# Performance work log

Hardware: AMD Instinct MI355X
Metric: run time of the kernel (lower is better)

Reference implementation:

```python
import jax, jax.numpy as jnp
import numpy as np

B, S, D, H = 4, 2048, 1024, 16
DK = D // H


def setup_inputs() -> dict:
    key = jax.random.key(0)
    ks = jax.random.split(key, 11)
    std = 1.0 / np.sqrt(D)
    mk = lambda k: jax.random.uniform(k, (D, D), jnp.float32, -std, std)
    mb = lambda k: jax.random.uniform(k, (D,), jnp.float32, -std, std)
    return {
        "query": jax.random.normal(ks[0], (B, S, D), jnp.float32),
        "key": jax.random.normal(ks[1], (B, S, D), jnp.float32),
        "value": jax.random.normal(ks[2], (B, S, D), jnp.float32),
        "Wq": mk(ks[3]), "bq": mb(ks[4]),
        "Wk": mk(ks[5]), "bk": mb(ks[6]),
        "Wv": mk(ks[7]), "bv": mb(ks[8]),
        "Wo": mk(ks[9]), "bo": mb(ks[10]),
    }


def reference(query, key, value, Wq, bq, Wk, bk, Wv, bv, Wo, bo):
    # Linear projections (torch Linear: x @ W.T + b)
    Q = query @ Wq.T + bq   # [B,S,D]
    K = key @ Wk.T + bk
    V = value @ Wv.T + bv
    # split heads -> [B,H,S,DK]
    Q = Q.reshape(B, S, H, DK).transpose(0, 2, 1, 3)
    K = K.reshape(B, S, H, DK).transpose(0, 2, 1, 3)
    V = V.reshape(B, S, H, DK).transpose(0, 2, 1, 3)
    scale = 1.0 / jnp.sqrt(jnp.asarray(DK, Q.dtype))
    scores = jnp.einsum("bhqd,bhkd->bhqk", Q, K) * scale  # [B,H,S,S]
    attn = jax.nn.softmax(scores, axis=-1)
    out = jnp.einsum("bhqk,bhkd->bhqd", attn, V)          # [B,H,S,DK]
    out = out.transpose(0, 2, 1, 3).reshape(B, S, D)       # [B,S,D]
    return out @ Wo.T + bo
```

## Files before the change

### kernel.cpp

```cpp
#include <hip/hip_runtime.h>
#include <hip/hip_bf16.h>
#include <stdint.h>


using f32x4  = __attribute__((ext_vector_type(4))) float;
using f32x16 = __attribute__((ext_vector_type(16))) float;
using s16x8  = __attribute__((ext_vector_type(8))) short;
using u16x8  = __attribute__((ext_vector_type(8))) unsigned short;
using u16x4  = __attribute__((ext_vector_type(4))) unsigned short;

#define MFMA16(a, b, c) __builtin_amdgcn_mfma_f32_16x16x32_bf16((a), (b), (c), 0, 0, 0)
#define MFMA32(a, b, c) __builtin_amdgcn_mfma_f32_32x32x16_bf16((a), (b), (c), 0, 0, 0)

#define GLL16(gptr, lptr)                                                      \
  __builtin_amdgcn_global_load_lds(                                            \
      (const __attribute__((address_space(1))) void*)(gptr),                   \
      (__attribute__((address_space(3))) void*)(lptr), 16, 0, 0)

__device__ __forceinline__ unsigned short f2bf(float f) {
  union { __hip_bfloat16 h; unsigned short u; } cv;
  cv.h = __float2bfloat16(f);
  return cv.u;
}

__device__ __forceinline__ unsigned int pkrne(float a, float b) {
  unsigned int ua = __builtin_bit_cast(unsigned int, a);
  unsigned int ub = __builtin_bit_cast(unsigned int, b);
  ua = ua + 0x7FFFu + ((ua >> 16) & 1u);
  ub = ub + 0x7FFFu + ((ub >> 16) & 1u);
  return __builtin_amdgcn_perm(ub, ua, 0x07060302u);
}

__device__ __forceinline__ float exp2a(float x) {
  return __builtin_amdgcn_exp2f(x);
}

__global__ __launch_bounds__(256) void cast_all_kernel(
    const float* __restrict__ wq, const float* __restrict__ wk,
    const float* __restrict__ wv, const float* __restrict__ wo,
    const float* __restrict__ xq, const float* __restrict__ xk,
    const float* __restrict__ xv, unsigned short* __restrict__ wbf,
    unsigned short* __restrict__ oxq, unsigned short* __restrict__ oxk,
    unsigned short* __restrict__ oxv) {
  const int job = blockIdx.y;
  const int i = blockIdx.x * 256 + threadIdx.x;
  const float* src;
  unsigned short* dst;
  size_t off;
  if (job < 4) {
    src = (job == 0) ? wq : (job == 1) ? wk : (job == 2) ? wv : wo;
    dst = wbf + (size_t)job * 1048576;
    off = (size_t)i;
  } else {
    const int xi = job - 4, z = xi >> 3, sl = xi & 7;
    src = (z == 0) ? xq : (z == 1) ? xk : xv;
    dst = (z == 0) ? oxq : (z == 1) ? oxk : oxv;
    off = (size_t)sl * 262144 + i;
  }
  float4 f = reinterpret_cast<const float4*>(src)[off];
  uint2 p;
  p.x = pkrne(f.x, f.y);
  p.y = pkrne(f.z, f.w);
  *reinterpret_cast<uint2*>(dst + off * 4) = p;
}

__global__ __launch_bounds__(256) void gemm_qkvv_kernel(
    const unsigned short* __restrict__ Xq, const unsigned short* __restrict__ Xk,
    const unsigned short* __restrict__ Xv, const unsigned short* __restrict__ wbf,
    const float* __restrict__ bq, const float* __restrict__ bk,
    const float* __restrict__ bv, unsigned short* __restrict__ Qh,
    unsigned short* __restrict__ Kh, unsigned short* __restrict__ Vh) {
  const int z = blockIdx.z;
  const unsigned short* Xbf = (z == 0) ? Xq : (z == 1) ? Xk : Xv;
  const unsigned short* W = wbf + (size_t)z * 1048576;
  const float* bias = (z == 0) ? bq : (z == 1) ? bk : bv;
  const float qscale = (z == 0) ? 0.18033688011112042f : 1.0f;

  __shared__ __align__(16) unsigned short Asm_[128 * 64];
  __shared__ __align__(16) unsigned short Bsm_[128 * 64];

  const int t = threadIdx.x;
  const int lane = t & 63, w = t >> 6;
  const int g = lane >> 4, c = lane & 15;
  const int wm = (w >> 1) * 64, wn = (w & 1) * 64;
  const int n0 = (blockIdx.y & 7) * 128;
  const int m0 = (blockIdx.x * 8 + (blockIdx.y >> 3)) * 128;

  f32x4 acc[4][4];
#pragma unroll
  for (int i = 0; i < 4; i++)
#pragma unroll
    for (int j = 0; j < 4; j++) acc[i][j] = (f32x4)0.0f;

  const int blr = lane >> 3;
  const int bgc = (lane & 7) ^ blr;

  for (int kt = 0; kt < 16; ++kt) {
    const int k0 = kt * 64;
    __syncthreads();
#pragma unroll
    for (int i = 0; i < 4; i++) {
      int ii = w * 4 + i;
      const unsigned short* ga = Xbf + (size_t)(m0 + ii * 8 + blr) * 1024 + k0 + bgc * 8;
      GLL16(ga, &Asm_[ii * 512]);
      const unsigned short* gb = W + (size_t)(n0 + ii * 8 + blr) * 1024 + k0 + bgc * 8;
      GLL16(gb, &Bsm_[ii * 512]);
    }
    __syncthreads();

#pragma unroll
    for (int ks = 0; ks < 2; ks++) {
      s16x8 af[4], bfr[4];
#pragma unroll
      for (int mt = 0; mt < 4; mt++) {
        int r = wm + mt * 16 + c;
        af[mt] = *reinterpret_cast<const s16x8*>(&Asm_[r * 64 + (((ks * 4 + g) ^ (c & 7)) << 3)]);
      }
#pragma unroll
      for (int nt = 0; nt < 4; nt++) {
        int r = wn + nt * 16 + c;
        bfr[nt] = *reinterpret_cast<const s16x8*>(&Bsm_[r * 64 + (((ks * 4 + g) ^ (c & 7)) << 3)]);
      }
      if (z == 2) {
#pragma unroll
        for (int nt = 0; nt < 4; nt++)
#pragma unroll
          for (int mt = 0; mt < 4; mt++)
            acc[nt][mt] = MFMA16(bfr[nt], af[mt], acc[nt][mt]);
      } else {
#pragma unroll
        for (int mt = 0; mt < 4; mt++)
#pragma unroll
          for (int nt = 0; nt < 4; nt++)
            acc[mt][nt] = MFMA16(af[mt], bfr[nt], acc[mt][nt]);
      }
    }
  }

  if (z == 2) {
#pragma unroll
    for (int nt = 0; nt < 4; nt++)
#pragma unroll
      for (int mt = 0; mt < 4; mt++) {
        int m = m0 + wm + mt * 16 + c;
        int b = m >> 11, s = m & 2047;
#pragma unroll
        for (int r = 0; r < 4; r++) {
          int n = n0 + wn + nt * 16 + g * 4 + r;
          int h = n >> 6, dk = n & 63;
          Vh[(((size_t)b * 16 + h) * 64 + dk) * 2048 + s] =
              f2bf(acc[nt][mt][r] + bv[n]);
        }
      }
  } else {
    unsigned short* dst = (z == 0) ? Qh : Kh;
#pragma unroll
    for (int mt = 0; mt < 4; mt++)
#pragma unroll
      for (int nt = 0; nt < 4; nt++) {
        int n = n0 + wn + nt * 16 + c;
        float bb = bias[n];
        int h = n >> 6, dk = n & 63;
#pragma unroll
        for (int r = 0; r < 4; r++) {
          int m = m0 + wm + mt * 16 + g * 4 + r;
          int b = m >> 11, s = m & 2047;
          dst[(((size_t)b * 16 + h) * 2048 + s) * 64 + dk] =
              f2bf((acc[mt][nt][r] + bb) * qscale);
        }
      }
  }
}

__global__ __launch_bounds__(256) void gemm_out_kernel(
    const unsigned short* __restrict__ AO, const unsigned short* __restrict__ Wo,
    const float* __restrict__ bo, float* __restrict__ out) {
  __shared__ __align__(16) unsigned short Asm_[128 * 64];
  __shared__ __align__(16) unsigned short Bsm_[64 * 64];

  const int t = threadIdx.x;
  const int lane = t & 63, w = t >> 6;
  const int g = lane >> 4, c = lane & 15;
  const int wm = (w >> 1) * 64, wn = (w & 1) * 32;
  const int n0 = (blockIdx.y & 15) * 64;
  const int m0 = (blockIdx.x * 8 + (blockIdx.y >> 4)) * 128;

  f32x4 acc[4][2];
#pragma unroll
  for (int i = 0; i < 4; i++)
#pragma unroll
    for (int j = 0; j < 2; j++) acc[i][j] = (f32x4)0.0f;

  const int blr = lane >> 3;
  const int bgc = (lane & 7) ^ blr;

  for (int kt = 0; kt < 16; ++kt) {
    const int k0 = kt * 64;
    __syncthreads();
#pragma unroll
    for (int i = 0; i < 4; i++) {
      int ii = w * 4 + i;
      const unsigned short* ga = AO + (size_t)(m0 + ii * 8 + blr) * 1024 + k0 + bgc * 8;
      GLL16(ga, &Asm_[ii * 512]);
    }
#pragma unroll
    for (int i = 0; i < 2; i++) {
      int ii = w * 2 + i;
      const unsigned short* gb = Wo + (size_t)(n0 + ii * 8 + blr) * 1024 + k0 + bgc * 8;
      GLL16(gb, &Bsm_[ii * 512]);
    }
    __syncthreads();

#pragma unroll
    for (int ks = 0; ks < 2; ks++) {
      s16x8 af[4], bfr[2];
#pragma unroll
      for (int mt = 0; mt < 4; mt++) {
        int r = wm + mt * 16 + c;
        af[mt] = *reinterpret_cast<const s16x8*>(&Asm_[r * 64 + (((ks * 4 + g) ^ (c & 7)) << 3)]);
      }
#pragma unroll
      for (int nt = 0; nt < 2; nt++) {
        int r = wn + nt * 16 + c;
        bfr[nt] = *reinterpret_cast<const s16x8*>(&Bsm_[r * 64 + (((ks * 4 + g) ^ (c & 7)) << 3)]);
      }
#pragma unroll
      for (int mt = 0; mt < 4; mt++)
#pragma unroll
        for (int nt = 0; nt < 2; nt++)
          acc[mt][nt] = MFMA16(af[mt], bfr[nt], acc[mt][nt]);
    }
  }

#pragma unroll
  for (int mt = 0; mt < 4; mt++)
#pragma unroll
    for (int nt = 0; nt < 2; nt++) {
      int n = n0 + wn + nt * 16 + c;
      float bb = bo[n];
#pragma unroll
      for (int r = 0; r < 4; r++) {
        int m = m0 + wm + mt * 16 + g * 4 + r;
        out[(size_t)m * 1024 + n] = acc[mt][nt][r] + bb;
      }
    }
}

__global__ __launch_bounds__(512) void attn_kernel(
    const unsigned short* __restrict__ Qh, const unsigned short* __restrict__ Kh,
    const unsigned short* __restrict__ Vh, unsigned short* __restrict__ AO) {
  const int bh = blockIdx.x * 8 + (blockIdx.y >> 3);
  const int b = bh >> 4, h = bh & 15;
  const int q0 = (blockIdx.y & 7) * 256;
  const int t = threadIdx.x, lane = t & 63, w = t >> 6;
  const int lo = lane & 31, hi = lane >> 5;

  __shared__ __align__(16) unsigned short Ks[2][64 * 64];
  __shared__ __align__(16) unsigned short Vs[2][64 * 64];

  const size_t kvbase = (size_t)bh * 2048 * 64;

  s16x8 qb[4];
  {
    const unsigned short* qp = Qh + kvbase + (size_t)(q0 + w * 32 + lo) * 64;
#pragma unroll
    for (int ks = 0; ks < 4; ks++)
      qb[ks] = *reinterpret_cast<const s16x8*>(qp + ks * 16 + hi * 8);
  }

  s16x8 onesb;
  {
    uint4 u;
    u.x = 0x3F803F80u; u.y = 0x3F803F80u; u.z = 0x3F803F80u; u.w = 0x3F803F80u;
    onesb = *reinterpret_cast<const s16x8*>(&u);
  }

  f32x16 oacc[2], lacc;
  oacc[0] = (f32x16)0.0f; oacc[1] = (f32x16)0.0f; lacc = (f32x16)0.0f;

  const int srow = t >> 3;
  const int gch = (t & 7) ^ (srow & 7) ^ w;
  const unsigned short* Kg = Kh + kvbase + (size_t)srow * 64 + gch * 8;
  const unsigned short* Vg = Vh + kvbase + (size_t)srow * 2048 + gch * 8;

  const int rx0 = (lo & 7) ^ (lo >> 3);
  const int rx1 = (lo & 7) ^ (4 | (lo >> 3));

  GLL16(Kg, &Ks[0][w * 512]);
  GLL16(Vg, &Vs[0][w * 512]);
  __syncthreads();

  for (int it = 0; it < 32; ++it) {
    const int cur = it & 1;
    if (it < 31) {
      const int kv = (it + 1) * 64;
      GLL16(Kg + (size_t)kv * 64, &Ks[cur ^ 1][w * 512]);
      GLL16(Vg + kv, &Vs[cur ^ 1][w * 512]);
    }

    f32x16 st[2];
    st[0] = (f32x16)0.0f; st[1] = (f32x16)0.0f;
#pragma unroll
    for (int kb = 0; kb < 2; kb++) {
      const int rx = kb ? rx1 : rx0;
#pragma unroll
      for (int ks = 0; ks < 4; ks++) {
        s16x8 ka = *reinterpret_cast<const s16x8*>(
            &Ks[cur][(kb * 32 + lo) * 64 + (((ks * 2 + hi) ^ rx) << 3)]);
        st[kb] = MFMA32(ka, qb[ks], st[kb]);
      }
    }

    s16x8 pa[4];
#pragma unroll
    for (int kb = 0; kb < 2; kb++) {
      float e[16];
#pragma unroll
      for (int r = 0; r < 16; r++) e[r] = exp2a(st[kb][r]);
#pragma unroll
      for (int half = 0; half < 2; half++) {
        const float* eb = e + half * 8;
        unsigned int x1 = pkrne(eb[0], eb[1]);
        unsigned int x2 = pkrne(eb[2], eb[3]);
        unsigned int y1 = pkrne(eb[4], eb[5]);
        unsigned int y2 = pkrne(eb[6], eb[7]);
        asm volatile("v_permlane32_swap_b32 %0, %1" : "+v"(x1), "+v"(y1));
        asm volatile("v_permlane32_swap_b32 %0, %1" : "+v"(x2), "+v"(y2));
        uint4 u;
        u.x = x1; u.y = x2; u.z = y1; u.w = y2;
        pa[kb * 2 + half] = *reinterpret_cast<const s16x8*>(&u);
      }
    }

#pragma unroll
    for (int ks = 0; ks < 4; ks++) lacc = MFMA32(pa[ks], onesb, lacc);

#pragma unroll
    for (int ks = 0; ks < 4; ks++)
#pragma unroll
      for (int db = 0; db < 2; db++) {
        const int rx = db ? rx1 : rx0;
        s16x8 vb = *reinterpret_cast<const s16x8*>(
            &Vs[cur][(db * 32 + lo) * 64 + (((ks * 2 + hi) ^ rx) << 3)]);
        oacc[db] = MFMA32(pa[ks], vb, oacc[db]);
      }

    __syncthreads();
  }

#pragma unroll
  for (int r = 0; r < 16; r++) {
    float inv_r = 1.0f / lacc[r];
    int qr = (r & 3) + ((r >> 2) << 3) + (hi << 2);
    int srow_q = q0 + w * 32 + qr;
    size_t obase = ((size_t)b * 2048 + srow_q) * 1024 + (size_t)h * 64;
    AO[obase + lo]      = f2bf(oacc[0][r] * inv_r);
    AO[obase + 32 + lo] = f2bf(oacc[1][r] * inv_r);
  }
}

extern "C" void kernel_launch(void* const* d_in, const int* in_sizes, int n_in,
                              void* d_out, int out_size, void* d_ws, size_t ws_size,
                              hipStream_t stream) {
  const float* query = (const float*)d_in[0];
  const float* key   = (const float*)d_in[1];
  const float* value = (const float*)d_in[2];
  const float* Wq = (const float*)d_in[3];
  const float* bq = (const float*)d_in[4];
  const float* Wk = (const float*)d_in[5];
  const float* bk = (const float*)d_in[6];
  const float* Wv = (const float*)d_in[7];
  const float* bv = (const float*)d_in[8];
  const float* Wo = (const float*)d_in[9];
  const float* bo = (const float*)d_in[10];

  uint8_t* wsb = (uint8_t*)d_ws;
  unsigned short* wbf = (unsigned short*)wsb;
  unsigned short* Qh  = (unsigned short*)(wsb + 8388608);
  unsigned short* Kh  = (unsigned short*)(wsb + 8388608 + 16777216);
  unsigned short* Vh  = (unsigned short*)(wsb + 8388608 + 2 * 16777216);
  unsigned short* AO  = (unsigned short*)(wsb + 8388608 + 3 * 16777216);
  unsigned short* Xq = AO;
  unsigned short* Xk = (unsigned short*)d_out;
  unsigned short* Xv = (unsigned short*)d_out + 8388608;

  cast_all_kernel<<<dim3(1024, 28), dim3(256), 0, stream>>>(
      Wq, Wk, Wv, Wo, query, key, value, wbf, Xq, Xk, Xv);
  gemm_qkvv_kernel<<<dim3(8, 64, 3), dim3(256), 0, stream>>>(
      Xq, Xk, Xv, wbf, bq, bk, bv, Qh, Kh, Vh);
  attn_kernel<<<dim3(8, 64), dim3(512), 0, stream>>>(Qh, Kh, Vh, AO);
  gemm_out_kernel<<<dim3(8, 128), dim3(256), 0, stream>>>(
      AO, wbf + (size_t)3 * 1048576, bo, (float*)d_out);
}
```

Measured before the change: 206.9 us.

## Split attention KV range across two blocks and combine partial outputs

Attention now runs on a grid with a z dimension of 2. Each block processes half of the key/value sequence and writes an unnormalized bf16 partial output and its row sums into scratch buffers, which reuse the output and weight workspaces. A new combine kernel adds the two partials and divides by the summed row normalizers to produce the attention output. This doubles the number of blocks so more work can be in flight. The cost is an extra kernel launch, extra global memory traffic for the partials, and an additional bf16 rounding of the unnormalized partial outputs.

```diff
diff --git a/kernel.cpp b/kernel.cpp
--- a/kernel.cpp
+++ b/kernel.cpp
@@ -29,6 +29,10 @@
   ua = ua + 0x7FFFu + ((ua >> 16) & 1u);
   ub = ub + 0x7FFFu + ((ub >> 16) & 1u);
   return __builtin_amdgcn_perm(ub, ua, 0x07060302u);
+}
+
+__device__ __forceinline__ float bf2f(unsigned short u) {
+  return __builtin_bit_cast(float, (unsigned int)u << 16);
 }
 
 __device__ __forceinline__ float exp2a(float x) {
@@ -248,10 +252,12 @@
 
 __global__ __launch_bounds__(512) void attn_kernel(
     const unsigned short* __restrict__ Qh, const unsigned short* __restrict__ Kh,
-    const unsigned short* __restrict__ Vh, unsigned short* __restrict__ AO) {
+    const unsigned short* __restrict__ Vh, unsigned short* __restrict__ Opart,
+    float* __restrict__ lw) {
   const int bh = blockIdx.x * 8 + (blockIdx.y >> 3);
   const int b = bh >> 4, h = bh & 15;
   const int q0 = (blockIdx.y & 7) * 256;
+  const int kvh = blockIdx.z;
   const int t = threadIdx.x, lane = t & 63, w = t >> 6;
   const int lo = lane & 31, hi = lane >> 5;
 
@@ -286,16 +292,18 @@
   const int rx0 = (lo & 7) ^ (lo >> 3);
   const int rx1 = (lo & 7) ^ (4 | (lo >> 3));
 
-  GLL16(Kg, &Ks[0][w * 512]);
-  GLL16(Vg, &Vs[0][w * 512]);
+  const int t0 = kvh * 16;
+
+  GLL16(Kg + (size_t)t0 * 4096, &Ks[0][w * 512]);
+  GLL16(Vg + t0 * 64, &Vs[0][w * 512]);
   __syncthreads();
 
-  for (int it = 0; it < 32; ++it) {
+  for (int it = 0; it < 16; ++it) {
     const int cur = it & 1;
-    if (it < 31) {
-      const int kv = (it + 1) * 64;
-      GLL16(Kg + (size_t)kv * 64, &Ks[cur ^ 1][w * 512]);
-      GLL16(Vg + kv, &Vs[cur ^ 1][w * 512]);
+    if (it < 15) {
+      const int tile = t0 + it + 1;
+      GLL16(Kg + (size_t)tile * 4096, &Ks[cur ^ 1][w * 512]);
+      GLL16(Vg + tile * 64, &Vs[cur ^ 1][w * 512]);
     }
 
     f32x16 st[2];
@@ -348,15 +356,40 @@
     __syncthreads();
   }
 
+  unsigned short* Op = Opart + (size_t)kvh * 8388608;
+  float* lp = lw + ((size_t)kvh << 17);
 #pragma unroll
   for (int r = 0; r < 16; r++) {
-    float inv_r = 1.0f / lacc[r];
     int qr = (r & 3) + ((r >> 2) << 3) + (hi << 2);
     int srow_q = q0 + w * 32 + qr;
     size_t obase = ((size_t)b * 2048 + srow_q) * 1024 + (size_t)h * 64;
-    AO[obase + lo]      = f2bf(oacc[0][r] * inv_r);
-    AO[obase + 32 + lo] = f2bf(oacc[1][r] * inv_r);
-  }
+    Op[obase + lo]      = f2bf(oacc[0][r]);
+    Op[obase + 32 + lo] = f2bf(oacc[1][r]);
+    if (lo == 0) lp[(size_t)bh * 2048 + srow_q] = lacc[r];
+  }
+}
+
+__global__ __launch_bounds__(256) void combine_kernel(
+    const unsigned short* __restrict__ O1, const unsigned short* __restrict__ O2,
+    const float* __restrict__ l1, const float* __restrict__ l2,
+    unsigned short* __restrict__ AO) {
+  size_t i = ((size_t)blockIdx.x * 256 + threadIdx.x) * 8;
+  int d = (int)(i & 1023);
+  int s = (int)((i >> 10) & 2047);
+  int b = (int)(i >> 21);
+  int h = d >> 6;
+  size_t li = ((size_t)(b * 16 + h) << 11) + s;
+  float inv = 1.0f / (l1[li] + l2[li]);
+  u16x8 a = *reinterpret_cast<const u16x8*>(O1 + i);
+  u16x8 c = *reinterpret_cast<const u16x8*>(O2 + i);
+  u16x8 o;
+#pragma unroll
+  for (int j = 0; j < 8; j++) {
+    float fa = __builtin_bit_cast(float, (unsigned int)a[j] << 16);
+    float fc = __builtin_bit_cast(float, (unsigned int)c[j] << 16);
+    o[j] = f2bf((fa + fc) * inv);
+  }
+  *reinterpret_cast<u16x8*>(AO + i) = o;
 }
 
 extern "C" void kernel_launch(void* const* d_in, const int* in_sizes, int n_in,
@@ -383,12 +416,16 @@
   unsigned short* Xq = AO;
   unsigned short* Xk = (unsigned short*)d_out;
   unsigned short* Xv = (unsigned short*)d_out + 8388608;
+  unsigned short* Opart = (unsigned short*)d_out;
+  float* lw = (float*)wbf;
 
   cast_all_kernel<<<dim3(1024, 28), dim3(256), 0, stream>>>(
       Wq, Wk, Wv, Wo, query, key, value, wbf, Xq, Xk, Xv);
   gemm_qkvv_kernel<<<dim3(8, 64, 3), dim3(256), 0, stream>>>(
       Xq, Xk, Xv, wbf, bq, bk, bv, Qh, Kh, Vh);
-  attn_kernel<<<dim3(8, 64), dim3(512), 0, stream>>>(Qh, Kh, Vh, AO);
+  attn_kernel<<<dim3(8, 64, 2), dim3(512), 0, stream>>>(Qh, Kh, Vh, Opart, lw);
+  combine_kernel<<<dim3(4096), dim3(256), 0, stream>>>(
+      Opart, Opart + 8388608, lw, lw + 131072, AO);
   gemm_out_kernel<<<dim3(8, 128), dim3(256), 0, stream>>>(
       AO, wbf + (size_t)3 * 1048576, bo, (float*)d_out);
 }
```

Result: slower. 216.5 us (+4.6%).
